# Kernel optimization log

Hardware: AMD Instinct MI355X
Metric: run time of the kernel (lower is better)

Reference implementation:

```python
import jax, jax.numpy as jnp
import numpy as np

HIDDEN = 768
OUT_DIM = 128
IN_DIM = OUT_DIM + 1  # LSTM input_size = output_dim + 1
T, B = 512, 256


def setup_inputs() -> dict:
    key = jax.random.key(0)
    ks = jax.random.split(key, 8)
    s = 1.0 / np.sqrt(HIDDEN)  # torch LSTM/Linear init scale
    seq = jax.random.normal(ks[0], (T, B, IN_DIM), dtype=jnp.float32)
    W_ih = jax.random.uniform(ks[1], (4 * HIDDEN, IN_DIM), minval=-s, maxval=s, dtype=jnp.float32)
    W_hh = jax.random.uniform(ks[2], (4 * HIDDEN, HIDDEN), minval=-s, maxval=s, dtype=jnp.float32)
    b_ih = jax.random.uniform(ks[3], (4 * HIDDEN,), minval=-s, maxval=s, dtype=jnp.float32)
    b_hh = jax.random.uniform(ks[4], (4 * HIDDEN,), minval=-s, maxval=s, dtype=jnp.float32)
    W_dec = jax.random.uniform(ks[5], (OUT_DIM, HIDDEN), minval=-s, maxval=s, dtype=jnp.float32)
    b_dec = jax.random.uniform(ks[6], (OUT_DIM,), minval=-s, maxval=s, dtype=jnp.float32)
    return {"sequence": seq, "W_ih": W_ih, "W_hh": W_hh, "b_ih": b_ih,
            "b_hh": b_hh, "W_dec": W_dec, "b_dec": b_dec}


def _lstm(sequence, W_ih, W_hh, b_ih, b_hh):
    # Pre-compute input projections for all timesteps in one big GEMM: [T,B,4H]
    x_proj = jnp.einsum('tbd,gd->tbg', sequence, W_ih) + (b_ih + b_hh)
    H = W_hh.shape[1]

    def step(carry, xp_t):
        h, c = carry
        gates = xp_t + h @ W_hh.T                      # [B,4H]
        i, f, g, o = jnp.split(gates, 4, axis=-1)      # torch gate order i,f,g,o
        i = jax.nn.sigmoid(i)
        f = jax.nn.sigmoid(f)
        g = jnp.tanh(g)
        o = jax.nn.sigmoid(o)
        c = f * c + i * g
        h = o * jnp.tanh(c)
        return (h, c), h

    Bsz = sequence.shape[1]
    h0 = jnp.zeros((Bsz, H), dtype=sequence.dtype)
    c0 = jnp.zeros((Bsz, H), dtype=sequence.dtype)
    (h_t, c_t), hidden_seq = jax.lax.scan(step, (h0, c0), x_proj)
    return hidden_seq, h_t, c_t


def reference(sequence, W_ih, W_hh, b_ih, b_hh, W_dec, b_dec):
    length = sequence.shape[0] // 2
    hidden_seq, h_t, c_t = _lstm(sequence, W_ih, W_hh, b_ih, b_hh)
    # decode the second (readout) half of the sequence; dropout is identity in eval
    out = jnp.einsum('tbh,oh->tbo', hidden_seq[length:], W_dec) + b_dec
    return out
```

## Files before the change

kernel.cpp:

```cpp
#include <hip/hip_runtime.h>
#include <cstdint>
#include <cstddef>

#define TT 512
#define BB 256
#define HID 768
#define INDIM 129
#define OUTD 128
#define KS_TOT 58
#define KS_REC 48
#define XSTR 168
#define GSTR 100

typedef __attribute__((ext_vector_type(8))) short bf16x8;
typedef __attribute__((ext_vector_type(4))) float f32x4;
typedef __attribute__((ext_vector_type(16))) float f32x16;
typedef unsigned short u16;
typedef unsigned long long u64;

#define MFMA32(A, B, C) __builtin_amdgcn_mfma_f32_32x32x16_bf16(A, B, C, 0, 0, 0)
#define ZERO16 {0.f,0.f,0.f,0.f,0.f,0.f,0.f,0.f,0.f,0.f,0.f,0.f,0.f,0.f,0.f,0.f}

__device__ __forceinline__ u16 f2bf(float f) {
  union { float f; unsigned u; } v; v.f = f;
  unsigned u = v.u;
  u += 0x7fffu + ((u >> 16) & 1u);
  return (u16)(u >> 16);
}
__device__ __forceinline__ float sigm(float x) { return 1.0f / (1.0f + __expf(-x)); }
__device__ __forceinline__ float tanh_fast(float x) { return 2.0f / (1.0f + __expf(-2.0f * x)) - 1.0f; }

__global__ __launch_bounds__(256) void prep_kernel(
    const float* __restrict__ W_ih, const float* __restrict__ W_hh,
    const float* __restrict__ b_ih, const float* __restrict__ b_hh,
    const float* __restrict__ W_dec, const float* __restrict__ b_dec,
    u16* __restrict__ Wpack, u16* __restrict__ Wdpack,
    float* __restrict__ biasg, u16* __restrict__ h0,
    unsigned* __restrict__ flags, float* __restrict__ out) {
  const int stride = blockDim.x * gridDim.x;
  const int i0 = blockIdx.x * blockDim.x + threadIdx.x;

  for (int i = i0; i < 32 * 3 * KS_TOT * 512; i += stride) {
    int jj = i & 7, lane = (i >> 3) & 63, r = i >> 9;
    int ks = r % KS_TOT; int r2 = r / KS_TOT;
    int nt = r2 % 3, ct = r2 / 3;
    int p = nt * 32 + (lane & 31);
    int g = p / 24, j = p - g * 24;
    int row = g * HID + ct * 24 + j;
    int kh = (lane >> 5) * 8 + jj;
    float v;
    if (ks < KS_REC) v = W_hh[(size_t)row * HID + ks * 16 + kh];
    else { int d = (ks - KS_REC) * 16 + kh; v = (d < INDIM) ? W_ih[(size_t)row * INDIM + d] : 0.f; }
    Wpack[i] = f2bf(v);
  }
  for (int i = i0; i < 4 * 48 * 512; i += stride) {
    int jj = i & 7, lane = (i >> 3) & 63, r = i >> 9;
    int ks = r % 48, nt = r / 48;
    int orow = nt * 32 + (lane & 31);
    int k = ks * 16 + (lane >> 5) * 8 + jj;
    Wdpack[i] = f2bf(W_dec[(size_t)orow * HID + k]);
  }
  for (int i = i0; i < 4 * HID; i += stride) biasg[i] = b_ih[i] + b_hh[i];
  for (int i = i0; i < BB * HID; i += stride) h0[i] = (u16)0;
  for (int i = i0; i < 1280; i += stride) flags[i] = 0u;
  for (int i = i0; i < 256 * BB * OUTD; i += stride) out[i] = b_dec[i & (OUTD - 1)];
}

__device__ __forceinline__ void waitflags(unsigned* fl, unsigned target, int lane) {
  for (;;) {
    unsigned v = __hip_atomic_load(&fl[lane & 31], __ATOMIC_RELAXED, __HIP_MEMORY_SCOPE_AGENT);
    if (__all((int)(v >= target))) break;
    __builtin_amdgcn_s_sleep(1);
  }
}
__device__ __forceinline__ unsigned flagld(const unsigned* p) {
  unsigned v; u64 a = (u64)p;
  asm volatile("global_load_dword %0, %1, off sc0 sc1\n\ts_waitcnt vmcnt(0)"
               : "=v"(v) : "v"(a) : "memory");
  return v;
}
__device__ __forceinline__ void stflag(unsigned* p, unsigned v) {
  u64 a = (u64)p;
  asm volatile("global_store_dword %0, %1, off sc0 sc1" :: "v"(a), "v"(v) : "memory");
}

#define HLD(i, off) asm volatile( \
    "global_load_dwordx4 %0, %1, off offset:" #off " sc0 sc1" \
    : "=v"(hreg[i]) : "v"(hrow) : "memory")
#define HLOADS() do { HLD(0,0); HLD(1,32); HLD(2,64); HLD(3,96); \
    HLD(4,128); HLD(5,160); HLD(6,192); HLD(7,224); \
    HLD(8,256); HLD(9,288); HLD(10,320); HLD(11,352); } while (0)

#define VMWAIT(n) do { asm volatile("s_waitcnt vmcnt(" #n ")" ::: "memory"); \
    __builtin_amdgcn_sched_barrier(0); } while (0)

__global__ __launch_bounds__(256, 1) void lstm_persist(
    const float* __restrict__ seq, const u16* __restrict__ Wpack,
    const u16* __restrict__ Wdpack, const float* __restrict__ biasg,
    u16* __restrict__ hb0, u16* __restrict__ hb1,
    unsigned* __restrict__ sflags, unsigned* __restrict__ fflags,
    float* __restrict__ out) {
  __shared__ float gbuf[4][32 * GSTR];
  __shared__ u16 xlds[32 * XSTR];
  __shared__ float biasl[96];

  const int tid = threadIdx.x;
  const int w = tid >> 6;
  const int lane = tid & 63;
  const int l5 = lane & 31;
  const int hi = lane >> 5;
  const int bid = blockIdx.x;
  const int bt = bid >> 5;
  const int ct = bid & 31;
  const int b0 = bt * 32;
  unsigned* sfl = sflags + bt * 128;
  unsigned* ffl = fflags + bt * 32;

  for (int i = tid; i < 32 * 31; i += 256) {
    int r = i / 31, d = INDIM + i - r * 31;
    xlds[r * XSTR + d] = (u16)0;
  }
  if (tid < 96) biasl[tid] = biasg[(tid / 24) * HID + ct * 24 + (tid % 24)];

  bf16x8 Breg[3][12];
  #pragma unroll
  for (int t = 0; t < 12; ++t)
    #pragma unroll
    for (int nt = 0; nt < 3; ++nt)
      Breg[nt][t] = *(const bf16x8*)(Wpack +
          (((size_t)(ct * 3 + nt)) * KS_TOT + (w * 12 + t)) * 512 + (size_t)lane * 8);

  const int icnt = (w < 2) ? 3 : 2;
  const int ioff = (w <= 2) ? w * 3 : 8;
  bf16x8 Bireg[3][3] = {};
  #pragma unroll
  for (int u = 0; u < 3; ++u)
    if (u < icnt) {
      #pragma unroll
      for (int nt = 0; nt < 3; ++nt)
        Bireg[u][nt] = *(const bf16x8*)(Wpack +
            (((size_t)(ct * 3 + nt)) * KS_TOT + KS_REC + ioff + u) * 512 + (size_t)lane * 8);
    }

  bf16x8 Dreg[12];
  #pragma unroll
  for (int t = 0; t < 12; ++t)
    Dreg[t] = *(const bf16x8*)(Wdpack +
        (((size_t)(ct & 3) * 48 + w * 12 + t) * 64 + lane) * 8);

  {
    const float* xs = seq + (size_t)b0 * INDIM;
    for (int i = tid; i < 32 * INDIM; i += 256) {
      int r = i / INDIM, d = i - r * INDIM;
      xlds[r * XSTR + d] = f2bf(xs[i]);
    }
  }

  float creg[4] = {0.f, 0.f, 0.f, 0.f};
  const int cr = tid / 6, cg = tid - (tid / 6) * 6;
  const unsigned* sfp = sfl + ((lane < 24) ? ((8 * w + lane / 3) * 4 + (lane % 3))
                                           : (8 * w) * 4);

  __syncthreads();

  for (int s = 0; s < TT; ++s) {
    const u16* hbprev = (s & 1) ? hb1 : hb0;
    u16* hbnext       = (s & 1) ? hb0 : hb1;

    for (;;) {
      unsigned v = flagld(sfp);
      if (__all((int)(v >= (unsigned)s))) break;
      __builtin_amdgcn_s_sleep(1);
    }

    bf16x8 hreg[12];
    {
      const u64 hrow = (u64)(hbprev + (size_t)(b0 + l5) * HID + w * 192 + hi * 8);
      HLOADS();
    }

    f32x16 acc[3] = {ZERO16, ZERO16, ZERO16};
    #pragma unroll
    for (int u = 0; u < 3; ++u)
      if (u < icnt) {
        int kk = ioff + u;
        bf16x8 a = *(const bf16x8*)(xlds + l5 * XSTR + kk * 16 + hi * 8);
        acc[0] = MFMA32(a, Bireg[u][0], acc[0]);
        acc[1] = MFMA32(a, Bireg[u][1], acc[1]);
        acc[2] = MFMA32(a, Bireg[u][2], acc[2]);
      }

    VMWAIT(6);
    #pragma unroll
    for (int t = 0; t < 6; ++t) {
      acc[0] = MFMA32(hreg[t], Breg[0][t], acc[0]);
      acc[1] = MFMA32(hreg[t], Breg[1][t], acc[1]);
      acc[2] = MFMA32(hreg[t], Breg[2][t], acc[2]);
    }
    VMWAIT(0);
    #pragma unroll
    for (int t = 6; t < 12; ++t) {
      acc[0] = MFMA32(hreg[t], Breg[0][t], acc[0]);
      acc[1] = MFMA32(hreg[t], Breg[1][t], acc[1]);
      acc[2] = MFMA32(hreg[t], Breg[2][t], acc[2]);
    }

    float xf[17];
    if (s + 1 < TT) {
      const float* xs = seq + ((size_t)(s + 1) * BB + b0) * INDIM;
      #pragma unroll
      for (int k = 0; k < 17; ++k) {
        int i = tid + k * 256;
        xf[k] = (i < 32 * INDIM) ? xs[i] : 0.f;
      }
    }

    {
      float* gbw = &gbuf[w][0];
      #pragma unroll
      for (int nt = 0; nt < 3; ++nt)
        #pragma unroll
        for (int r = 0; r < 16; ++r) {
          int row = (r & 3) + 8 * (r >> 2) + 4 * hi;
          gbw[row * GSTR + nt * 32 + l5] = acc[nt][r];
        }
    }

    __syncthreads();

    if (tid < 192) {
      float gv4[4][4];
      #pragma unroll
      for (int g = 0; g < 4; ++g) {
        f32x4 v = *(f32x4*)&gbuf[0][cr * GSTR + g * 24 + cg * 4];
        #pragma unroll
        for (int w2 = 1; w2 < 4; ++w2)
          v += *(f32x4*)&gbuf[w2][cr * GSTR + g * 24 + cg * 4];
        #pragma unroll
        for (int e = 0; e < 4; ++e) gv4[g][e] = v[e] + biasl[g * 24 + cg * 4 + e];
      }
      u64 pack = 0;
      #pragma unroll
      for (int e = 0; e < 4; ++e) {
        float iv = sigm(gv4[0][e]), fv2 = sigm(gv4[1][e]);
        float gg = tanh_fast(gv4[2][e]), ov = sigm(gv4[3][e]);
        float cn = fv2 * creg[e] + iv * gg;
        creg[e] = cn;
        pack |= (u64)f2bf(ov * tanh_fast(cn)) << (16 * e);
      }
      __hip_atomic_store((u64*)hbnext + ((size_t)(b0 + cr) * HID + ct * 24 + cg * 4) / 4,
                         pack, __ATOMIC_RELAXED, __HIP_MEMORY_SCOPE_AGENT);
      asm volatile("s_waitcnt vmcnt(0)" ::: "memory");
      __builtin_amdgcn_sched_barrier(0);
      if (lane == 0) stflag(sfl + ct * 4 + w, (unsigned)(s + 1));
    }

    if (s + 1 < TT) {
      #pragma unroll
      for (int k = 0; k < 17; ++k) {
        int i = tid + k * 256;
        if (i < 32 * INDIM) {
          int r = i / INDIM, d = i - r * INDIM;
          xlds[r * XSTR + d] = f2bf(xf[k]);
        }
      }
    }

    if (s >= 257 && ((ct >> 2) == ((s - 257) & 7))) {
      const int ont = ct & 3;
      f32x16 dacc = ZERO16;
      #pragma unroll
      for (int t = 0; t < 12; ++t) dacc = MFMA32(hreg[t], Dreg[t], dacc);
      float* ob = out + ((size_t)(s - 257) * BB + b0) * OUTD + ont * 32;
      #pragma unroll
      for (int r = 0; r < 16; ++r) {
        int row = (r & 3) + 8 * (r >> 2) + 4 * hi;
        atomicAdd(&ob[(size_t)row * OUTD + l5], dacc[r]);
      }
    }

    __syncthreads();
  }

  if (tid == 0) stflag(ffl + ct, (unsigned)TT);

  if ((ct >> 2) == 7) {
    waitflags(ffl, (unsigned)TT, lane);
    const int ont = ct & 3;
    bf16x8 hreg[12];
    {
      const u64 hrow = (u64)(hb0 + (size_t)(b0 + l5) * HID + w * 192 + hi * 8);
      HLOADS();
    }
    VMWAIT(0);
    f32x16 dacc = ZERO16;
    #pragma unroll
    for (int t = 0; t < 12; ++t) dacc = MFMA32(hreg[t], Dreg[t], dacc);
    float* ob = out + ((size_t)255 * BB + b0) * OUTD + ont * 32;
    #pragma unroll
    for (int r = 0; r < 16; ++r) {
      int row = (r & 3) + 8 * (r >> 2) + 4 * hi;
      atomicAdd(&ob[(size_t)row * OUTD + l5], dacc[r]);
    }
  }
}

extern "C" void kernel_launch(void* const* d_in, const int* in_sizes, int n_in,
                              void* d_out, int out_size, void* d_ws, size_t ws_size,
                              hipStream_t stream) {
  (void)in_sizes; (void)n_in; (void)out_size; (void)ws_size;
  const float* seq   = (const float*)d_in[0];
  const float* W_ih  = (const float*)d_in[1];
  const float* W_hh  = (const float*)d_in[2];
  const float* b_ih  = (const float*)d_in[3];
  const float* b_hh  = (const float*)d_in[4];
  const float* W_dec = (const float*)d_in[5];
  const float* b_dec = (const float*)d_in[6];
  float* out = (float*)d_out;

  u16* Wpack  = (u16*)d_ws;
  u16* Wdpack = Wpack + 32 * 3 * KS_TOT * 512;
  u16* h0     = Wdpack + 4 * 48 * 512;
  u16* h1     = h0 + BB * HID;
  float* biasg = (float*)(h1 + BB * HID);
  unsigned* sflags = (unsigned*)(biasg + 4 * HID);
  unsigned* fflags = sflags + 1024;

  prep_kernel<<<2048, 256, 0, stream>>>(W_ih, W_hh, b_ih, b_hh, W_dec, b_dec,
                                        Wpack, Wdpack, biasg, h0, sflags, out);
  lstm_persist<<<256, 256, 0, stream>>>(seq, Wpack, Wdpack, biasg,
                                        h0, h1, sflags, fflags, out);
}
```

Baseline: 2.884 ms.

## Reduce decoder partials in LDS and overlap first input MFMA with flag wait

The decoder output is now reduced across the four waves in shared memory and written once with vector stores that include the bias. This replaces 16 global atomicAdds per lane and drops the prep pass that pre-filled the output with the bias. The first input-projection MFMA group is also hoisted ahead of the spin-wait on step flags, so it can overlap the synchronisation latency. The cost is extra LDS and an extra read of the shared buffer after the block barrier on duty steps. It also assumes icnt is at least 1, since the first MFMA group now runs unconditionally.

Measured after the change: 2.883 ms. No clear change (-0.0%).

```diff
diff --git a/kernel.cpp b/kernel.cpp
--- a/kernel.cpp
+++ b/kernel.cpp
@@ -11,6 +11,7 @@
 #define KS_REC 48
 #define XSTR 168
 #define GSTR 100
+#define DSTR 36
 
 typedef __attribute__((ext_vector_type(8))) short bf16x8;
 typedef __attribute__((ext_vector_type(4))) float f32x4;
@@ -37,6 +38,7 @@
     u16* __restrict__ Wpack, u16* __restrict__ Wdpack,
     float* __restrict__ biasg, u16* __restrict__ h0,
     unsigned* __restrict__ flags, float* __restrict__ out) {
+  (void)b_dec; (void)out;
   const int stride = blockDim.x * gridDim.x;
   const int i0 = blockIdx.x * blockDim.x + threadIdx.x;
 
@@ -63,7 +65,6 @@
   for (int i = i0; i < 4 * HID; i += stride) biasg[i] = b_ih[i] + b_hh[i];
   for (int i = i0; i < BB * HID; i += stride) h0[i] = (u16)0;
   for (int i = i0; i < 1280; i += stride) flags[i] = 0u;
-  for (int i = i0; i < 256 * BB * OUTD; i += stride) out[i] = b_dec[i & (OUTD - 1)];
 }
 
 __device__ __forceinline__ void waitflags(unsigned* fl, unsigned target, int lane) {
@@ -97,10 +98,12 @@
 __global__ __launch_bounds__(256, 1) void lstm_persist(
     const float* __restrict__ seq, const u16* __restrict__ Wpack,
     const u16* __restrict__ Wdpack, const float* __restrict__ biasg,
+    const float* __restrict__ b_dec,
     u16* __restrict__ hb0, u16* __restrict__ hb1,
     unsigned* __restrict__ sflags, unsigned* __restrict__ fflags,
     float* __restrict__ out) {
   __shared__ float gbuf[4][32 * GSTR];
+  __shared__ float dbuf[4][32 * DSTR];
   __shared__ u16 xlds[32 * XSTR];
   __shared__ float biasl[96];
 
@@ -160,12 +163,24 @@
   const int cr = tid / 6, cg = tid - (tid / 6) * 6;
   const unsigned* sfp = sfl + ((lane < 24) ? ((8 * w + lane / 3) * 4 + (lane % 3))
                                            : (8 * w) * 4);
+  const int srow = tid >> 3, sc4 = (tid & 7) * 4;
+  const int ont = ct & 3;
 
   __syncthreads();
 
   for (int s = 0; s < TT; ++s) {
     const u16* hbprev = (s & 1) ? hb1 : hb0;
     u16* hbnext       = (s & 1) ? hb0 : hb1;
+    const bool duty = (s >= 257) && ((ct >> 2) == ((s - 257) & 7));
+
+    f32x16 acc[3] = {ZERO16, ZERO16, ZERO16};
+    {
+      int kk = ioff;
+      bf16x8 a = *(const bf16x8*)(xlds + l5 * XSTR + kk * 16 + hi * 8);
+      acc[0] = MFMA32(a, Bireg[0][0], acc[0]);
+      acc[1] = MFMA32(a, Bireg[0][1], acc[1]);
+      acc[2] = MFMA32(a, Bireg[0][2], acc[2]);
+    }
 
     for (;;) {
       unsigned v = flagld(sfp);
@@ -179,9 +194,8 @@
       HLOADS();
     }
 
-    f32x16 acc[3] = {ZERO16, ZERO16, ZERO16};
-    #pragma unroll
-    for (int u = 0; u < 3; ++u)
+    #pragma unroll
+    for (int u = 1; u < 3; ++u)
       if (u < icnt) {
         int kk = ioff + u;
         bf16x8 a = *(const bf16x8*)(xlds + l5 * XSTR + kk * 16 + hi * 8);
@@ -266,27 +280,36 @@
       }
     }
 
-    if (s >= 257 && ((ct >> 2) == ((s - 257) & 7))) {
-      const int ont = ct & 3;
+    if (duty) {
       f32x16 dacc = ZERO16;
       #pragma unroll
       for (int t = 0; t < 12; ++t) dacc = MFMA32(hreg[t], Dreg[t], dacc);
-      float* ob = out + ((size_t)(s - 257) * BB + b0) * OUTD + ont * 32;
+      float* db = &dbuf[w][0];
       #pragma unroll
       for (int r = 0; r < 16; ++r) {
         int row = (r & 3) + 8 * (r >> 2) + 4 * hi;
-        atomicAdd(&ob[(size_t)row * OUTD + l5], dacc[r]);
+        db[row * DSTR + l5] = dacc[r];
       }
     }
 
     __syncthreads();
+
+    if (duty) {
+      const int t0 = s - 257;
+      f32x4 v = *(f32x4*)&dbuf[0][srow * DSTR + sc4];
+      #pragma unroll
+      for (int w2 = 1; w2 < 4; ++w2)
+        v += *(f32x4*)&dbuf[w2][srow * DSTR + sc4];
+      #pragma unroll
+      for (int e = 0; e < 4; ++e) v[e] += b_dec[ont * 32 + sc4 + e];
+      *(f32x4*)&out[((size_t)t0 * BB + b0 + srow) * OUTD + ont * 32 + sc4] = v;
+    }
   }
 
   if (tid == 0) stflag(ffl + ct, (unsigned)TT);
 
   if ((ct >> 2) == 7) {
     waitflags(ffl, (unsigned)TT, lane);
-    const int ont = ct & 3;
     bf16x8 hreg[12];
     {
       const u64 hrow = (u64)(hb0 + (size_t)(b0 + l5) * HID + w * 192 + hi * 8);
@@ -296,12 +319,20 @@
     f32x16 dacc = ZERO16;
     #pragma unroll
     for (int t = 0; t < 12; ++t) dacc = MFMA32(hreg[t], Dreg[t], dacc);
-    float* ob = out + ((size_t)255 * BB + b0) * OUTD + ont * 32;
+    float* db = &dbuf[w][0];
     #pragma unroll
     for (int r = 0; r < 16; ++r) {
       int row = (r & 3) + 8 * (r >> 2) + 4 * hi;
-      atomicAdd(&ob[(size_t)row * OUTD + l5], dacc[r]);
-    }
+      db[row * DSTR + l5] = dacc[r];
+    }
+    __syncthreads();
+    f32x4 v = *(f32x4*)&dbuf[0][srow * DSTR + sc4];
+    #pragma unroll
+    for (int w2 = 1; w2 < 4; ++w2)
+      v += *(f32x4*)&dbuf[w2][srow * DSTR + sc4];
+    #pragma unroll
+    for (int e = 0; e < 4; ++e) v[e] += b_dec[ont * 32 + sc4 + e];
+    *(f32x4*)&out[((size_t)255 * BB + b0 + srow) * OUTD + ont * 32 + sc4] = v;
   }
 }
 
@@ -328,6 +359,6 @@
 
   prep_kernel<<<2048, 256, 0, stream>>>(W_ih, W_hh, b_ih, b_hh, W_dec, b_dec,
                                         Wpack, Wdpack, biasg, h0, sflags, out);
-  lstm_persist<<<256, 256, 0, stream>>>(seq, Wpack, Wdpack, biasg,
+  lstm_persist<<<256, 256, 0, stream>>>(seq, Wpack, Wdpack, biasg, b_dec,
                                         h0, h1, sflags, fflags, out);
 }
```
